# Kernel optimization log

Hardware: AMD Instinct MI355X
Metric: run time of the kernel (lower is better)

## Reference

```python
import jax, jax.numpy as jnp
import numpy as np

N, E, IN, H, HEADS, L, OUT = 4096, 262144, 64, 128, 4, 2, 2
DH = H // HEADS  # 32, per-head dim for both GAT and global MHA
BN_EPS = 1e-5
NEG_SLOPE = 0.2  # GATConv leaky_relu default


def setup_inputs() -> dict:
    key = jax.random.key(0)
    ks = iter(jax.random.split(key, 32))
    rn = lambda shape, s: jax.random.normal(next(ks), shape, jnp.float32) * s
    return {
        "x": rn((N, IN), 1.0),
        "edge_index": jax.random.randint(next(ks), (2, E), 0, N),
        "w_in": rn((H, IN), IN ** -0.5),
        "b_in": rn((H,), 0.02),
        "w_gat": rn((L, H, H), H ** -0.5),
        "att_src": rn((L, HEADS, DH), 0.1),
        "att_dst": rn((L, HEADS, DH), 0.1),
        "b_gat": rn((L, H), 0.02),
        "w_qkv": rn((L, 3 * H, H), H ** -0.5),
        "b_qkv": rn((L, 3 * H), 0.02),
        "w_o": rn((L, H, H), H ** -0.5),
        "b_o": rn((L, H), 0.02),
        "bn_gamma": 1.0 + rn((L, 3, H), 0.05),
        "bn_beta": rn((L, 3, H), 0.05),
        "w1": rn((L, 2 * H, H), H ** -0.5),
        "b1": rn((L, 2 * H), 0.02),
        "w2": rn((L, H, 2 * H), (2 * H) ** -0.5),
        "b2": rn((L, H), 0.02),
        "w_out": rn((OUT, H), H ** -0.5),
        "b_out": rn((OUT,), 0.02),
    }


def _bn(h, g, b):
    # eval-mode BatchNorm1d with running_mean=0, running_var=1
    return h * (g / jnp.sqrt(1.0 + BN_EPS)) + b


def _gat(x, src, dst, w, a_src, a_dst, bias):
    # GATConv(hidden, hidden//heads, heads=HEADS, add_self_loops=False), concat=True
    xp = (x @ w.T).reshape(N, HEADS, DH)                  # [N, HEADS, DH]
    al_s = jnp.einsum('nhd,hd->nh', xp, a_src)            # [N, HEADS]
    al_d = jnp.einsum('nhd,hd->nh', xp, a_dst)
    logit = al_s[src] + al_d[dst]                         # [E, HEADS]
    logit = jnp.where(logit >= 0, logit, NEG_SLOPE * logit)
    m = jax.ops.segment_max(logit, dst, num_segments=N)   # scatter-softmax over dst
    m = jnp.where(jnp.isfinite(m), m, 0.0)
    e = jnp.exp(logit - m[dst])
    denom = jax.ops.segment_sum(e, dst, num_segments=N)
    alpha = e / (denom[dst] + 1e-16)
    out = jax.ops.segment_sum(alpha[:, :, None] * xp[src], dst, num_segments=N)
    return out.reshape(N, H) + bias


def _mha(x, wqkv, bqkv, wo, bo):
    # torch.nn.MultiheadAttention self-attention over all N nodes (one graph)
    qkv = x @ wqkv.T + bqkv
    q, k, v = jnp.split(qkv, 3, axis=-1)
    q = q.reshape(N, HEADS, DH)
    k = k.reshape(N, HEADS, DH)
    v = v.reshape(N, HEADS, DH)
    scores = jnp.einsum('nhd,mhd->hnm', q, k) / jnp.sqrt(jnp.float32(DH))
    attn = jax.nn.softmax(scores, axis=-1)
    out = jnp.einsum('hnm,mhd->nhd', attn, v).reshape(N, H)
    return out @ wo.T + bo


def reference(x, edge_index, w_in, b_in, w_gat, att_src, att_dst, b_gat,
              w_qkv, b_qkv, w_o, b_o, bn_gamma, bn_beta,
              w1, b1, w2, b2, w_out, b_out):
    src, dst = edge_index[0], edge_index[1]
    h = jax.nn.relu(x @ w_in.T + b_in)
    for l in range(L):
        # GPSConv: local GAT branch (dropout inactive in eval)
        h_loc = _gat(h, src, dst, w_gat[l], att_src[l], att_dst[l], b_gat[l]) + h
        h_loc = _bn(h_loc, bn_gamma[l, 0], bn_beta[l, 0])
        # GPSConv: global attention branch
        h_att = _mha(h, w_qkv[l], b_qkv[l], w_o[l], b_o[l]) + h
        h_att = _bn(h_att, bn_gamma[l, 1], bn_beta[l, 1])
        out = h_loc + h_att
        mlp = jax.nn.relu(out @ w1[l].T + b1[l]) @ w2[l].T + b2[l]
        out = _bn(out + mlp, bn_gamma[l, 2], bn_beta[l, 2])
        # GPSRiskModel residual + relu (dropout inactive in eval)
        h = jax.nn.relu(out + h)
    return h @ w_out.T + b_out
```

## Files before the change

kernel.cpp:

```cpp
#include <hip/hip_runtime.h>

#define NN 4096
#define EE 262144
#define INF_ 64
#define HH 128
#define HEADS 4
#define DH 32
#define LL 2
#define NH (NN * HH)
#define KSPLIT 16
#define L2E 1.4426950408889634f

typedef unsigned short u16;
typedef unsigned int u32;
using bf16x8 = __attribute__((ext_vector_type(8))) short;
using f32x4 = __attribute__((ext_vector_type(4))) float;

__device__ __forceinline__ float bf2f(u16 v) { return __uint_as_float(((u32)v) << 16); }
__device__ __forceinline__ u16 f2bf(float f) {
    u32 u = __float_as_uint(f);
    u32 r = (u + 0x7fffu + ((u >> 16) & 1u)) >> 16;
    return (u16)r;
}
__device__ __forceinline__ u32 encf(float f) {
    u32 b = __float_as_uint(f);
    return (b & 0x80000000u) ? ~b : (b | 0x80000000u);
}
__device__ __forceinline__ float decf(u32 u) {
    u32 b = (u & 0x80000000u) ? (u & 0x7fffffffu) : ~u;
    return __uint_as_float(b);
}

__global__ __launch_bounds__(256) void k_detect(const u16* __restrict__ x, int* __restrict__ flag,
                                                int* __restrict__ cnt, u32* __restrict__ gmax) {
    int t = threadIdx.x;
    for (int i = t; i < NN; i += 256) cnt[i] = 0;
    if (t < 16) gmax[t] = 0;
    __shared__ int cs[256];
    u16 v = x[2 * t];
    int e = (v >> 7) & 0xFF;
    cs[t] = (e >= 100 && e <= 140) ? 1 : 0;
    __syncthreads();
    for (int s = 128; s > 0; s >>= 1) {
        if (t < s) cs[t] += cs[t + s];
        __syncthreads();
    }
    if (t == 0) *flag = (cs[0] >= 128) ? 1 : 0;
}

#define MAXSEG 16
struct SegF { const void* src[MAXSEG]; int dst[MAXSEG]; int n[MAXSEG]; int cnt; };
struct SegB { const void* src[8]; u16* dst[8]; u16* dst2[8]; int n[8]; int cnt; };
__global__ __launch_bounds__(256) void k_prep(SegF SF, float* __restrict__ W, SegB SB,
                                              const int* __restrict__ flag,
                                              const int* __restrict__ dst, int* __restrict__ cnt) {
    int bid = blockIdx.x, t = threadIdx.x;
    if (bid < 96) {
        int seg = bid >> 3, bx = bid & 7;
        if (seg >= SF.cnt) return;
        int n = SF.n[seg];
        float* d = W + SF.dst[seg];
        const void* s = SF.src[seg];
        int f = *flag;
        for (int i = bx * 256 + t; i < n; i += 8 * 256)
            d[i] = f ? bf2f(((const u16*)s)[i]) : ((const float*)s)[i];
    } else if (bid < 992) {
        int b2 = bid - 96;
        int seg = b2 >> 7, bx = b2 & 127;
        if (seg >= SB.cnt) return;
        int f = *flag;
        u16* d = SB.dst[seg];
        u16* d2 = SB.dst2[seg];
        if (f && !d2) return;
        int n = SB.n[seg];
        const void* s = SB.src[seg];
        for (int i = bx * 256 + t; i < n; i += 128 * 256) {
            if (d2) {
                float v = f ? bf2f(((const u16*)s)[i]) : ((const float*)s)[i];
                u16 h = f2bf(v);
                d[i] = h;
                d2[i] = f2bf(v - bf2f(h));
            } else {
                d[i] = f2bf(((const float*)s)[i]);
            }
        }
    } else {
        int e = (bid - 992) * 256 + t;
        if (e < EE) atomicAdd(&cnt[dst[e]], 1);
    }
}

__global__ __launch_bounds__(128) void k_mgemm(const u16* __restrict__ Ahi, const u16* __restrict__ Alo,
                                               const u16* __restrict__ Wc, const u16* __restrict__ Wd,
                                               const int* __restrict__ flag,
                                               const float* __restrict__ bias,
                                               float* __restrict__ outf, u16* __restrict__ outb16,
                                               u16* __restrict__ outhi, u16* __restrict__ outlo,
                                               int K, int J, int relu, int jtiles,
                                               const int* __restrict__ scnt, int* __restrict__ srowstart,
                                               int* __restrict__ scursor) {
    __shared__ int part[128];
    if ((int)blockIdx.y >= jtiles) {
        if (blockIdx.x != 0 || scnt == nullptr) return;
        int t = threadIdx.x;
        int loc[32];
        int s = 0;
#pragma unroll
        for (int i = 0; i < 32; ++i) { loc[i] = s; s += scnt[t * 32 + i]; }
        part[t] = s;
        __syncthreads();
        for (int off = 1; off < 128; off <<= 1) {
            int v = part[t];
            int a = (t >= off) ? part[t - off] : 0;
            __syncthreads();
            part[t] = v + a;
            __syncthreads();
        }
        int base = (t == 0) ? 0 : part[t - 1];
#pragma unroll
        for (int i = 0; i < 32; ++i) {
            srowstart[t * 32 + i] = base + loc[i];
            scursor[t * 32 + i] = base + loc[i];
        }
        return;
    }
    const u16* Wb = (*flag) ? Wd : Wc;
    int wave = threadIdx.x >> 6, lane = threadIdx.x & 63;
    int grp = lane >> 4, lcol = lane & 15;
    int m0 = blockIdx.x * 32 + wave * 16;
    int j0 = blockIdx.y * 64;
    f32x4 acc[4];
#pragma unroll
    for (int s = 0; s < 4; ++s) acc[s] = (f32x4){0.f, 0.f, 0.f, 0.f};
    const u16* ah = Ahi + (size_t)(m0 + lcol) * K + grp * 8;
    const u16* al = Alo + (size_t)(m0 + lcol) * K + grp * 8;
    const u16* wb = Wb + (size_t)(j0 + lcol) * K + grp * 8;
    for (int k = 0; k < K; k += 32) {
        bf16x8 va = *(const bf16x8*)(ah + k);
        bf16x8 vl = *(const bf16x8*)(al + k);
#pragma unroll
        for (int s = 0; s < 4; ++s) {
            bf16x8 vw = *(const bf16x8*)(wb + (size_t)s * 16 * K + k);
            acc[s] = __builtin_amdgcn_mfma_f32_16x16x32_bf16(va, vw, acc[s], 0, 0, 0);
            acc[s] = __builtin_amdgcn_mfma_f32_16x16x32_bf16(vl, vw, acc[s], 0, 0, 0);
        }
    }
#pragma unroll
    for (int s = 0; s < 4; ++s) {
        int col = j0 + s * 16 + lcol;
        float bs = bias ? bias[col] : 0.f;
#pragma unroll
        for (int r = 0; r < 4; ++r) {
            float v = acc[s][r] + bs;
            if (relu) v = fmaxf(v, 0.f);
            size_t idx = (size_t)(m0 + grp * 4 + r) * J + col;
            if (outf) outf[idx] = v;
            if (outb16) outb16[idx] = f2bf(v);
            if (outhi) {
                u16 hv = f2bf(v);
                outhi[idx] = hv;
                outlo[idx] = f2bf(v - bf2f(hv));
            }
        }
    }
}

__global__ __launch_bounds__(128) void k_gemm_gq(const u16* __restrict__ Ahi, const u16* __restrict__ Alo,
                                                 const u16* __restrict__ wgatc, const u16* __restrict__ wgatd,
                                                 const u16* __restrict__ wqkvc, const u16* __restrict__ wqkvd,
                                                 const int* __restrict__ flag,
                                                 const float* __restrict__ bqkv,
                                                 u16* __restrict__ xpb, u16* __restrict__ qkvb,
                                                 const int* __restrict__ esrc_src, const int* __restrict__ esrc_dst,
                                                 int* __restrict__ cursor, int* __restrict__ esrc) {
    if (blockIdx.y >= 8) {
        int b = (blockIdx.y - 8) * 128 + blockIdx.x;
        for (int e = b * 128 + threadIdx.x; e < EE; e += 32768) {
            int d = esrc_dst[e];
            int p = atomicAdd(&cursor[d], 1);
            esrc[p] = esrc_src[e];
        }
        return;
    }
    int wave = threadIdx.x >> 6, lane = threadIdx.x & 63;
    int grp = lane >> 4, lcol = lane & 15;
    int m0 = blockIdx.x * 32 + wave * 16;
    int jb = blockIdx.y;
    int j0 = jb * 64;
    int f = *flag;
    const u16* wgat = f ? wgatd : wgatc;
    const u16* wqkv = f ? wqkvd : wqkvc;
    const u16* Wb = (jb < 2) ? (wgat + (size_t)j0 * HH) : (wqkv + (size_t)(j0 - 128) * HH);
    f32x4 acc[4];
#pragma unroll
    for (int s = 0; s < 4; ++s) acc[s] = (f32x4){0.f, 0.f, 0.f, 0.f};
    const u16* ah = Ahi + (size_t)(m0 + lcol) * HH + grp * 8;
    const u16* al = Alo + (size_t)(m0 + lcol) * HH + grp * 8;
    const u16* wb = Wb + (size_t)lcol * HH + grp * 8;
    for (int k = 0; k < HH; k += 32) {
        bf16x8 va = *(const bf16x8*)(ah + k);
        bf16x8 vl = *(const bf16x8*)(al + k);
#pragma unroll
        for (int s = 0; s < 4; ++s) {
            bf16x8 vw = *(const bf16x8*)(wb + (size_t)s * 16 * HH + k);
            acc[s] = __builtin_amdgcn_mfma_f32_16x16x32_bf16(va, vw, acc[s], 0, 0, 0);
            acc[s] = __builtin_amdgcn_mfma_f32_16x16x32_bf16(vl, vw, acc[s], 0, 0, 0);
        }
    }
    if (jb < 2) {
#pragma unroll
        for (int s = 0; s < 4; ++s) {
            int col = j0 + s * 16 + lcol;
#pragma unroll
            for (int r = 0; r < 4; ++r)
                xpb[(size_t)(m0 + grp * 4 + r) * HH + col] = f2bf(acc[s][r]);
        }
    } else {
#pragma unroll
        for (int s = 0; s < 4; ++s) {
            int colq = j0 - 128 + s * 16 + lcol;
            float bs = bqkv[colq];
#pragma unroll
            for (int r = 0; r < 4; ++r)
                qkvb[(size_t)(m0 + grp * 4 + r) * 384 + colq] = f2bf(acc[s][r] + bs);
        }
    }
}

__global__ __launch_bounds__(256) void k_womlp(const u16* __restrict__ Ahi, const u16* __restrict__ Alo,
                                               const u16* __restrict__ Woc, const u16* __restrict__ Wod,
                                               const u16* __restrict__ W1c, const u16* __restrict__ W1d,
                                               const u16* __restrict__ W2c, const u16* __restrict__ W2d,
                                               const int* __restrict__ flag,
                                               const float* __restrict__ bo, const float* __restrict__ b1,
                                               const float* __restrict__ b2,
                                               const float* __restrict__ gatb, const float* __restrict__ bgat,
                                               const float* __restrict__ gam, const float* __restrict__ bet,
                                               const float* __restrict__ gam2, const float* __restrict__ bet2,
                                               float* __restrict__ hbuf, u16* __restrict__ hhi,
                                               u16* __restrict__ hlo) {
    __shared__ float Of[16][132];
    __shared__ u16 A2hi[16][136], A2lo[16][136];
    __shared__ u16 Hhi[16][264], Hlo[16][264];
    int f = *flag;
    const u16* Wo = f ? Wod : Woc;
    const u16* W1 = f ? W1d : W1c;
    const u16* W2 = f ? W2d : W2c;
    int wave = threadIdx.x >> 6, lane = threadIdx.x & 63;
    int grp = lane >> 4, lcol = lane & 15;
    int m0 = blockIdx.x * 16;
    float rs = rsqrtf(1.00001f);

    {
        int j0 = wave * 32;
        f32x4 acc[2];
#pragma unroll
        for (int s = 0; s < 2; ++s) acc[s] = (f32x4){0.f, 0.f, 0.f, 0.f};
        const u16* ah = Ahi + (size_t)(m0 + lcol) * HH + grp * 8;
        const u16* al = Alo + (size_t)(m0 + lcol) * HH + grp * 8;
        const u16* wb = Wo + (size_t)(j0 + lcol) * HH + grp * 8;
#pragma unroll
        for (int k = 0; k < HH; k += 32) {
            bf16x8 va = *(const bf16x8*)(ah + k);
            bf16x8 vl = *(const bf16x8*)(al + k);
#pragma unroll
            for (int s = 0; s < 2; ++s) {
                bf16x8 vw = *(const bf16x8*)(wb + (size_t)s * 16 * HH + k);
                acc[s] = __builtin_amdgcn_mfma_f32_16x16x32_bf16(va, vw, acc[s], 0, 0, 0);
                acc[s] = __builtin_amdgcn_mfma_f32_16x16x32_bf16(vl, vw, acc[s], 0, 0, 0);
            }
        }
#pragma unroll
        for (int s = 0; s < 2; ++s) {
            int col = j0 + s * 16 + lcol;
            float bs = bo[col];
            float g0 = gam[col] * rs, b0 = bet[col];
            float g1 = gam[HH + col] * rs, bb1 = bet[HH + col];
            float bg = bgat[col];
#pragma unroll
            for (int r = 0; r < 4; ++r) {
                int row = grp * 4 + r;
                size_t idx = (size_t)(m0 + row) * HH + col;
                float proj = acc[s][r] + bs;
                float hv = hbuf[idx];
                float hl = g0 * (gatb[idx] + bg + hv) + b0;
                float ha = g1 * (proj + hv) + bb1;
                float v = hl + ha;
                Of[row][col] = v;
                u16 hb = f2bf(v);
                A2hi[row][col] = hb;
                A2lo[row][col] = f2bf(v - bf2f(hb));
            }
        }
    }
    __syncthreads();
    {
        int j0 = wave * 64;
        f32x4 acc[4];
#pragma unroll
        for (int s = 0; s < 4; ++s) acc[s] = (f32x4){0.f, 0.f, 0.f, 0.f};
        const u16* wb = W1 + (size_t)(j0 + lcol) * HH + grp * 8;
#pragma unroll
        for (int k = 0; k < HH; k += 32) {
            bf16x8 va = *(const bf16x8*)(&A2hi[lcol][k + grp * 8]);
            bf16x8 vl = *(const bf16x8*)(&A2lo[lcol][k + grp * 8]);
#pragma unroll
            for (int s = 0; s < 4; ++s) {
                bf16x8 vw = *(const bf16x8*)(wb + (size_t)s * 16 * HH + k);
                acc[s] = __builtin_amdgcn_mfma_f32_16x16x32_bf16(va, vw, acc[s], 0, 0, 0);
                acc[s] = __builtin_amdgcn_mfma_f32_16x16x32_bf16(vl, vw, acc[s], 0, 0, 0);
            }
        }
#pragma unroll
        for (int s = 0; s < 4; ++s) {
            int col = j0 + s * 16 + lcol;
            float bs = b1[col];
#pragma unroll
            for (int r = 0; r < 4; ++r) {
                float v = fmaxf(acc[s][r] + bs, 0.f);
                int row = grp * 4 + r;
                u16 hv = f2bf(v);
                Hhi[row][col] = hv;
                Hlo[row][col] = f2bf(v - bf2f(hv));
            }
        }
    }
    __syncthreads();
    {
        int j0 = wave * 32;
        f32x4 acc[2];
#pragma unroll
        for (int s = 0; s < 2; ++s) acc[s] = (f32x4){0.f, 0.f, 0.f, 0.f};
        const u16* wb = W2 + (size_t)(j0 + lcol) * 256 + grp * 8;
#pragma unroll
        for (int k = 0; k < 256; k += 32) {
            bf16x8 va = *(const bf16x8*)(&Hhi[lcol][k + grp * 8]);
            bf16x8 vl = *(const bf16x8*)(&Hlo[lcol][k + grp * 8]);
#pragma unroll
            for (int s = 0; s < 2; ++s) {
                bf16x8 vw = *(const bf16x8*)(wb + (size_t)s * 16 * 256 + k);
                acc[s] = __builtin_amdgcn_mfma_f32_16x16x32_bf16(va, vw, acc[s], 0, 0, 0);
                acc[s] = __builtin_amdgcn_mfma_f32_16x16x32_bf16(vl, vw, acc[s], 0, 0, 0);
            }
        }
#pragma unroll
        for (int s = 0; s < 2; ++s) {
            int col = j0 + s * 16 + lcol;
            float bs = b2[col];
            float g2 = gam2[col] * rs, bb2 = bet2[col];
#pragma unroll
            for (int r = 0; r < 4; ++r) {
                int row = grp * 4 + r;
                size_t idx = (size_t)(m0 + row) * HH + col;
                float mlpo = acc[s][r] + bs;
                float o2 = g2 * (Of[row][col] + mlpo) + bb2;
                float v = fmaxf(o2 + hbuf[idx], 0.f);
                hbuf[idx] = v;
                u16 hb = f2bf(v);
                hhi[idx] = hb;
                hlo[idx] = f2bf(v - bf2f(hb));
            }
        }
    }
}

__global__ __launch_bounds__(256) void k_splitlog(const u16* __restrict__ qkvb,
                                                  float* __restrict__ PM, float* __restrict__ PL,
                                                  u16* __restrict__ PO,
                                                  const u16* __restrict__ xpb,
                                                  const float* __restrict__ asrc,
                                                  const float* __restrict__ adst,
                                                  float* __restrict__ als, float* __restrict__ ald,
                                                  u32* __restrict__ gmax) {
    __shared__ __align__(16) u16 Klds[64][40];
    __shared__ __align__(16) u32 Vlds[32][40];
    __shared__ __align__(16) u16 Plds[4][32][36];

    if (blockIdx.x >= 2048) {
        float* red = (float*)&Klds[0][0];
        int t = (blockIdx.x - 2048) * 256 + threadIdx.x;
        int n = t >> 2, hh = t & 3;
        const u16* xr = xpb + (size_t)n * HH + hh * DH;
        float s1 = 0.f, s2 = 0.f;
#pragma unroll
        for (int d = 0; d < DH; ++d) {
            float v = bf2f(xr[d]);
            s1 += v * asrc[hh * DH + d];
            s2 += v * adst[hh * DH + d];
        }
        als[t] = s1;
        ald[t] = s2;
        int lt = threadIdx.x;
        red[lt] = s1;
        __syncthreads();
        for (int off = 128; off >= 4; off >>= 1) {
            if (lt < off) red[lt] = fmaxf(red[lt], red[lt + off]);
            __syncthreads();
        }
        if (lt < 4) atomicMax(&gmax[lt], encf(red[lt]));
        __syncthreads();
        red[lt] = s2;
        __syncthreads();
        for (int off = 128; off >= 4; off >>= 1) {
            if (lt < off) red[lt] = fmaxf(red[lt], red[lt + off]);
            __syncthreads();
        }
        if (lt < 4) atomicMax(&gmax[4 + lt], encf(red[lt]));
        return;
    }

    const float C1 = 0.17677669529663687f * L2E;
    int head = blockIdx.x & 3;
    int qt = (blockIdx.x >> 2) & 31;
    int ks = blockIdx.x >> 7;
    int tid = threadIdx.x;
    int wave = tid >> 6, lane = tid & 63;
    int grp = lane >> 4, lcol = lane & 15;

    int qrow0 = qt * 128 + wave * 32;
    bf16x8 aQ0 = *(const bf16x8*)(qkvb + (size_t)(qrow0 + lcol) * 384 + head * 32 + grp * 8);
    bf16x8 aQ1 = *(const bf16x8*)(qkvb + (size_t)(qrow0 + 16 + lcol) * 384 + head * 32 + grp * 8);

    short onev = (lcol == 0) ? (short)0x3F80 : (short)0;
    bf16x8 bOne = {onev, onev, onev, onev, onev, onev, onev, onev};

    f32x4 oc00 = {0.f, 0.f, 0.f, 0.f}, oc01 = {0.f, 0.f, 0.f, 0.f};
    f32x4 oc10 = {0.f, 0.f, 0.f, 0.f}, oc11 = {0.f, 0.f, 0.f, 0.f};
    f32x4 ol0 = {0.f, 0.f, 0.f, 0.f}, ol1 = {0.f, 0.f, 0.f, 0.f};
    float msh = -INFINITY;

    int isK = (tid < 128);
    int st = tid & 127;
    int skey = st >> 1, shalf = (st & 1) * 16;
    int vj = st & 15, vc = (st >> 4) & 1, dgrp = st >> 5;
    const u16* kptr = qkvb + 128 + head * 32 + shalf;
    const u16* vptr = qkvb + 256 + head * 32 + dgrp * 8;
    int vk0 = vc * 32 + vj;
    int vk1 = vc * 32 + 16 + vj;

    int kt0 = ks * (NN / KSPLIT);
    bf16x8 r0, r1;
    if (isK) {
        r0 = *(const bf16x8*)(kptr + (size_t)(kt0 + skey) * 384);
        r1 = *(const bf16x8*)(kptr + (size_t)(kt0 + skey) * 384 + 8);
    } else {
        r0 = *(const bf16x8*)(vptr + (size_t)(kt0 + vk0) * 384);
        r1 = *(const bf16x8*)(vptr + (size_t)(kt0 + vk1) * 384);
    }

    const int NT = (NN / KSPLIT) / 64;
    for (int t = 0; t < NT; ++t) {
        if (isK) {
            *(bf16x8*)(&Klds[skey][shalf]) = r0;
            *(bf16x8*)(&Klds[skey][shalf + 8]) = r1;
        } else {
#pragma unroll
            for (int j = 0; j < 8; ++j)
                Vlds[dgrp * 8 + j][vc * 20 + vj] = (u32)(u16)r0[j] | ((u32)(u16)r1[j] << 16);
        }
        __syncthreads();
        if (t + 1 < NT) {
            int kn = kt0 + (t + 1) * 64;
            if (isK) {
                r0 = *(const bf16x8*)(kptr + (size_t)(kn + skey) * 384);
                r1 = *(const bf16x8*)(kptr + (size_t)(kn + skey) * 384 + 8);
            } else {
                r0 = *(const bf16x8*)(vptr + (size_t)(kn + vk0) * 384);
                r1 = *(const bf16x8*)(vptr + (size_t)(kn + vk1) * 384);
            }
        }
        f32x4 sc0[4], sc1[4];
        f32x4 zero = {0.f, 0.f, 0.f, 0.f};
        __builtin_amdgcn_s_setprio(1);
#pragma unroll
        for (int s = 0; s < 4; ++s) {
            bf16x8 bK = *(const bf16x8*)(&Klds[s * 16 + lcol][grp * 8]);
            sc0[s] = __builtin_amdgcn_mfma_f32_16x16x32_bf16(aQ0, bK, zero, 0, 0, 0);
            sc1[s] = __builtin_amdgcn_mfma_f32_16x16x32_bf16(aQ1, bK, zero, 0, 0, 0);
        }
        __builtin_amdgcn_s_setprio(0);
        float mymax = sc0[0][0];
#pragma unroll
        for (int s = 0; s < 4; ++s)
#pragma unroll
            for (int r = 0; r < 4; ++r) {
                mymax = fmaxf(mymax, sc0[s][r]);
                mymax = fmaxf(mymax, sc1[s][r]);
            }
        mymax = fmaxf(mymax, __shfl_xor(mymax, 1));
        mymax = fmaxf(mymax, __shfl_xor(mymax, 2));
        mymax = fmaxf(mymax, __shfl_xor(mymax, 4));
        mymax = fmaxf(mymax, __shfl_xor(mymax, 8));
        float mnew = fmaxf(msh, mymax * C1);
        float cc = __builtin_exp2f(msh - mnew);
        msh = mnew;
        oc00 *= cc; oc01 *= cc; ol0 *= cc;
        oc10 *= cc; oc11 *= cc; ol1 *= cc;
#pragma unroll
        for (int c2 = 0; c2 < 2; ++c2) {
#pragma unroll
            for (int r = 0; r < 4; ++r) {
                float p0 = __builtin_exp2f(__builtin_fmaf(sc0[2 * c2][r], C1, -mnew));
                float p1 = __builtin_exp2f(__builtin_fmaf(sc0[2 * c2 + 1][r], C1, -mnew));
                *(u32*)(&Plds[wave][grp * 4 + r][2 * lcol]) =
                    __builtin_amdgcn_perm(__float_as_uint(p1), __float_as_uint(p0), 0x07060302u);
                float q0 = __builtin_exp2f(__builtin_fmaf(sc1[2 * c2][r], C1, -mnew));
                float q1 = __builtin_exp2f(__builtin_fmaf(sc1[2 * c2 + 1][r], C1, -mnew));
                *(u32*)(&Plds[wave][16 + grp * 4 + r][2 * lcol]) =
                    __builtin_amdgcn_perm(__float_as_uint(q1), __float_as_uint(q0), 0x07060302u);
            }
            bf16x8 aP0 = *(const bf16x8*)(&Plds[wave][lcol][grp * 8]);
            bf16x8 aP1 = *(const bf16x8*)(&Plds[wave][16 + lcol][grp * 8]);
            bf16x8 bV0 = *(const bf16x8*)(&Vlds[lcol][c2 * 20 + grp * 4]);
            bf16x8 bV1 = *(const bf16x8*)(&Vlds[16 + lcol][c2 * 20 + grp * 4]);
            __builtin_amdgcn_s_setprio(1);
            oc00 = __builtin_amdgcn_mfma_f32_16x16x32_bf16(aP0, bV0, oc00, 0, 0, 0);
            oc01 = __builtin_amdgcn_mfma_f32_16x16x32_bf16(aP0, bV1, oc01, 0, 0, 0);
            ol0 = __builtin_amdgcn_mfma_f32_16x16x32_bf16(aP0, bOne, ol0, 0, 0, 0);
            oc10 = __builtin_amdgcn_mfma_f32_16x16x32_bf16(aP1, bV0, oc10, 0, 0, 0);
            oc11 = __builtin_amdgcn_mfma_f32_16x16x32_bf16(aP1, bV1, oc11, 0, 0, 0);
            ol1 = __builtin_amdgcn_mfma_f32_16x16x32_bf16(aP1, bOne, ol1, 0, 0, 0);
            __builtin_amdgcn_s_setprio(0);
        }
        __syncthreads();
    }
#pragma unroll
    for (int r = 0; r < 4; ++r) {
        int row0 = qrow0 + grp * 4 + r;
        size_t b0 = ((size_t)row0 * HEADS + head) * KSPLIT + ks;
        PO[b0 * 32 + lcol] = f2bf(oc00[r]);
        PO[b0 * 32 + 16 + lcol] = f2bf(oc01[r]);
        int row1 = row0 + 16;
        size_t b1 = ((size_t)row1 * HEADS + head) * KSPLIT + ks;
        PO[b1 * 32 + lcol] = f2bf(oc10[r]);
        PO[b1 * 32 + 16 + lcol] = f2bf(oc11[r]);
        if (lcol == 0) {
            PM[b0] = msh;
            PL[b0] = ol0[r];
            PM[b1] = msh;
            PL[b1] = ol1[r];
        }
    }
}

#define GCHUNK 256
__global__ __launch_bounds__(128) void k_gatcomb(const int* __restrict__ esrc, const int* __restrict__ rowstart,
                                                 const int* __restrict__ cnt, const float* __restrict__ als,
                                                 const float* __restrict__ ald, const u16* __restrict__ xpb,
                                                 float* __restrict__ gatout, const u32* __restrict__ gmax,
                                                 const float* __restrict__ PM, const float* __restrict__ PL,
                                                 const u16* __restrict__ PO, u16* __restrict__ atthi,
                                                 u16* __restrict__ attlo) {
    __shared__ float red[512];
    __shared__ float elds[GCHUNK * 4];
    __shared__ int slds[GCHUNK];
    int t = threadIdx.x;

    if (blockIdx.x >= NN) {
        int n2 = blockIdx.x - NN;
        float* wn = red;
        if (t < 64) {
            int head = t >> 4, ks = t & 15;
            size_t b = ((size_t)n2 * HEADS + head) * KSPLIT + ks;
            float pm = PM[b];
            float m = pm;
#pragma unroll
            for (int off = 1; off < 16; off <<= 1) m = fmaxf(m, __shfl_xor(m, off));
            float w = __builtin_exp2f(pm - m);
            float lw = PL[b] * w;
#pragma unroll
            for (int off = 1; off < 16; off <<= 1) lw += __shfl_xor(lw, off);
            wn[t] = w / lw;
        }
        __syncthreads();
        int head = t >> 5, dim = t & 31;
        size_t b0 = ((size_t)n2 * HEADS + head) * KSPLIT;
        float o = 0.f;
#pragma unroll
        for (int k = 0; k < KSPLIT; ++k)
            o += wn[head * 16 + k] * bf2f(PO[(b0 + k) * 32 + dim]);
        size_t idx = (size_t)n2 * HH + t;
        u16 h = f2bf(o);
        atthi[idx] = h;
        attlo[idx] = f2bf(o - bf2f(h));
        return;
    }

    int n = blockIdx.x;
    int base = rowstart[n], c = cnt[n];
    float4 adv = ((const float4*)ald)[n];
    float ad[4] = {adv.x, adv.y, adv.z, adv.w};
    float M2[4];
#pragma unroll
    for (int h = 0; h < 4; ++h) {
        float bound = decf(gmax[h]) + decf(gmax[4 + h]);
        float M = bound >= 0.f ? bound : 0.2f * bound;
        M2[h] = M * L2E;
    }
    float dsum[4] = {0.f, 0.f, 0.f, 0.f};
    float acc = 0.f;
    int ht = t >> 5;
    for (int ch = 0; ch < c; ch += GCHUNK) {
        int cn = min(GCHUNK, c - ch);
        __syncthreads();
        for (int i = t; i < cn; i += 128) {
            int s = esrc[base + ch + i];
            slds[i] = s;
            float4 as = ((const float4*)als)[s];
            float lg, e;
            lg = as.x + ad[0]; lg = lg >= 0.f ? lg : 0.2f * lg; e = __builtin_exp2f(lg * L2E - M2[0]); elds[i * 4 + 0] = e; dsum[0] += e;
            lg = as.y + ad[1]; lg = lg >= 0.f ? lg : 0.2f * lg; e = __builtin_exp2f(lg * L2E - M2[1]); elds[i * 4 + 1] = e; dsum[1] += e;
            lg = as.z + ad[2]; lg = lg >= 0.f ? lg : 0.2f * lg; e = __builtin_exp2f(lg * L2E - M2[2]); elds[i * 4 + 2] = e; dsum[2] += e;
            lg = as.w + ad[3]; lg = lg >= 0.f ? lg : 0.2f * lg; e = __builtin_exp2f(lg * L2E - M2[3]); elds[i * 4 + 3] = e; dsum[3] += e;
        }
        __syncthreads();
        int i = 0;
        for (; i + 4 <= cn; i += 4) {
            int s0 = slds[i], s1 = slds[i + 1], s2 = slds[i + 2], s3 = slds[i + 3];
            float x0 = bf2f(xpb[(size_t)s0 * HH + t]);
            float x1 = bf2f(xpb[(size_t)s1 * HH + t]);
            float x2 = bf2f(xpb[(size_t)s2 * HH + t]);
            float x3 = bf2f(xpb[(size_t)s3 * HH + t]);
            acc += elds[i * 4 + ht] * x0 + elds[(i + 1) * 4 + ht] * x1;
            acc += elds[(i + 2) * 4 + ht] * x2 + elds[(i + 3) * 4 + ht] * x3;
        }
        for (; i < cn; ++i) acc += elds[i * 4 + ht] * bf2f(xpb[(size_t)slds[i] * HH + t]);
    }
    __syncthreads();
#pragma unroll
    for (int h = 0; h < 4; ++h) red[h * 128 + t] = dsum[h];
    __syncthreads();
    for (int s2 = 64; s2 > 0; s2 >>= 1) {
        if (t < s2) {
#pragma unroll
            for (int h = 0; h < 4; ++h)
                red[h * 128 + t] += red[h * 128 + t + s2];
        }
        __syncthreads();
    }
    float inv = 1.f / (red[ht * 128] + 1e-16f);
    gatout[(size_t)n * HH + t] = acc * inv;
}

__global__ __launch_bounds__(64) void k_out(const float* __restrict__ h, const float* __restrict__ w,
                                            const float* __restrict__ b, void* __restrict__ yout,
                                            const int* __restrict__ flag) {
    int n = blockIdx.x, l = threadIdx.x;
    float a0 = 0.f, a1 = 0.f;
    for (int k = l; k < HH; k += 64) {
        float hv = h[(size_t)n * HH + k];
        a0 += hv * w[k];
        a1 += hv * w[HH + k];
    }
#pragma unroll
    for (int off = 32; off > 0; off >>= 1) {
        a0 += __shfl_xor(a0, off);
        a1 += __shfl_xor(a1, off);
    }
    if (l == 0) {
        float o0 = a0 + b[0], o1 = a1 + b[1];
        if (*flag) {
            u16* y = (u16*)yout;
            y[n * 2 + 0] = f2bf(o0);
            y[n * 2 + 1] = f2bf(o1);
        } else {
            float* y = (float*)yout;
            y[n * 2 + 0] = o0;
            y[n * 2 + 1] = o1;
        }
    }
}

extern "C" void kernel_launch(void* const* d_in, const int* in_sizes, int n_in,
                              void* d_out, int out_size, void* d_ws, size_t ws_size,
                              hipStream_t stream) {
    float* W = (float*)d_ws;
    size_t o = 0;
    auto take = [&](size_t n) { size_t r = o; o += n; return r; };
    size_t pb_in = take(HH);
    size_t pattS = take(LL * HEADS * DH);
    size_t pattD = take(LL * HEADS * DH);
    size_t pb_gat = take(LL * HH);
    size_t pb_qkv = take(LL * 3 * HH);
    size_t pb_o  = take(LL * HH);
    size_t pbn_g = take(LL * 3 * HH);
    size_t pbn_b = take(LL * 3 * HH);
    size_t pb1   = take(LL * 2 * HH);
    size_t pb2   = take(LL * HH);
    size_t pw_out = take(2 * HH);
    size_t pb_out = take(2);
    auto takeb = [&](size_t nu16) { size_t r = o; o += (nu16 + 1) / 2; return r; };
    size_t bw_in  = takeb(HH * INF_);
    size_t bw_gat = takeb(LL * HH * HH);
    size_t bw_qkv = takeb(LL * 3 * HH * HH);
    size_t bw_o   = takeb(LL * HH * HH);
    size_t bw1    = takeb(LL * 2 * HH * HH);
    size_t bw2    = takeb(LL * HH * 2 * HH);
    o = (o + 127) & ~(size_t)127;
    size_t ohbuf = take(NH);
    size_t ogat  = take(NH);
    size_t oals  = take(NN * HEADS);
    size_t oald  = take(NN * HEADS);
    size_t opm   = take(NN * HEADS * KSPLIT);
    size_t opl   = take(NN * HEADS * KSPLIT);
    size_t opo   = takeb((size_t)NN * HEADS * KSPLIT * 32);
    size_t oqkvb = takeb(NN * 384);
    size_t oxpb  = takeb(NH);
    size_t oxhi  = takeb(NN * INF_);
    size_t oxlo  = takeb(NN * INF_);
    size_t ohhi  = takeb(NH);
    size_t ohlo  = takeb(NH);
    size_t oahi  = takeb(NH);
    size_t oalo  = takeb(NH);
    int* ibase    = (int*)(W + o);
    int* iflag    = ibase;
    int* cnt      = ibase + 64;
    int* rowstart = cnt + NN;
    int* cursor   = rowstart + NN;
    int* esrc     = cursor + NN;
    u32* gmax     = (u32*)(esrc + EE);

    float* hbuf = W + ohbuf;
    float* gatb = W + ogat;
    float* als  = W + oals;
    float* ald  = W + oald;
    float* pmb  = W + opm;
    float* plb  = W + opl;
    u16* pob  = (u16*)(W + opo);
    u16* qkvb = (u16*)(W + oqkvb);
    u16* xpb  = (u16*)(W + oxpb);
    u16* xhi = (u16*)(W + oxhi), *xlo = (u16*)(W + oxlo);
    u16* hhi = (u16*)(W + ohhi), *hlo = (u16*)(W + ohlo);
    u16* ahi = (u16*)(W + oahi), *alo = (u16*)(W + oalo);

    const int* src = (const int*)d_in[1];
    const int* dst = (const int*)d_in[1] + EE;
    const u16* dw_in  = (const u16*)d_in[2];
    const u16* dw_gat = (const u16*)d_in[4];
    const u16* dw_qkv = (const u16*)d_in[8];
    const u16* dw_o   = (const u16*)d_in[10];
    const u16* dw1    = (const u16*)d_in[14];
    const u16* dw2    = (const u16*)d_in[16];

    k_detect<<<1, 256, 0, stream>>>((const u16*)d_in[0], iflag, cnt, gmax);

    SegF SF = {};
    int nf = 0;
    auto addf = [&](int idx, size_t off, int n) { SF.src[nf] = d_in[idx]; SF.dst[nf] = (int)off; SF.n[nf] = n; ++nf; };
    addf(3, pb_in, HH);
    addf(5, pattS, LL * HEADS * DH);
    addf(6, pattD, LL * HEADS * DH);
    addf(7, pb_gat, LL * HH);
    addf(9, pb_qkv, LL * 3 * HH);
    addf(11, pb_o, LL * HH);
    addf(12, pbn_g, LL * 3 * HH);
    addf(13, pbn_b, LL * 3 * HH);
    addf(15, pb1, LL * 2 * HH);
    addf(17, pb2, LL * HH);
    addf(18, pw_out, 2 * HH);
    addf(19, pb_out, 2);
    SF.cnt = nf;

    SegB SB = {};
    int nb = 0;
    auto addb = [&](int idx, size_t off, int n, u16* d2) {
        SB.src[nb] = d_in[idx]; SB.dst[nb] = (u16*)(W + off); SB.dst2[nb] = d2; SB.n[nb] = n; ++nb;
    };
    addb(2, bw_in, HH * INF_, nullptr);
    addb(4, bw_gat, LL * HH * HH, nullptr);
    addb(8, bw_qkv, LL * 3 * HH * HH, nullptr);
    addb(10, bw_o, LL * HH * HH, nullptr);
    addb(14, bw1, LL * 2 * HH * HH, nullptr);
    addb(16, bw2, LL * HH * 2 * HH, nullptr);
    SB.src[nb] = d_in[0]; SB.dst[nb] = xhi; SB.dst2[nb] = xlo; SB.n[nb] = NN * INF_; ++nb;
    SB.cnt = nb;

    k_prep<<<2016, 256, 0, stream>>>(SF, W, SB, iflag, dst, cnt);

    k_mgemm<<<dim3(NN / 32, HH / 64 + 1), 128, 0, stream>>>(xhi, xlo, (u16*)(W + bw_in), dw_in, iflag,
                                                            W + pb_in, hbuf, nullptr, hhi, hlo, INF_, HH, 1,
                                                            HH / 64, cnt, rowstart, cursor);

    for (int l = 0; l < LL; ++l) {
        k_gemm_gq<<<dim3(NN / 32, (l == 0) ? 10 : 8), 128, 0, stream>>>(hhi, hlo,
                                                        (u16*)(W + bw_gat) + (size_t)l * HH * HH,
                                                        dw_gat + (size_t)l * HH * HH,
                                                        (u16*)(W + bw_qkv) + (size_t)l * 3 * HH * HH,
                                                        dw_qkv + (size_t)l * 3 * HH * HH,
                                                        iflag, W + pb_qkv + l * 3 * HH, xpb, qkvb,
                                                        src, dst, cursor, esrc);
        k_splitlog<<<2048 + (NN * HEADS) / 256, 256, 0, stream>>>(qkvb, pmb, plb, pob, xpb,
                                                                  W + pattS + l * HEADS * DH,
                                                                  W + pattD + l * HEADS * DH,
                                                                  als, ald, gmax + l * 8);
        k_gatcomb<<<2 * NN, 128, 0, stream>>>(esrc, rowstart, cnt, als, ald, xpb, gatb, gmax + l * 8,
                                              pmb, plb, pob, ahi, alo);
        k_womlp<<<NN / 16, 256, 0, stream>>>(ahi, alo,
                                             (u16*)(W + bw_o) + (size_t)l * HH * HH,
                                             dw_o + (size_t)l * HH * HH,
                                             (u16*)(W + bw1) + (size_t)l * 2 * HH * HH,
                                             dw1 + (size_t)l * 2 * HH * HH,
                                             (u16*)(W + bw2) + (size_t)l * HH * 2 * HH,
                                             dw2 + (size_t)l * HH * 2 * HH, iflag,
                                             W + pb_o + l * HH, W + pb1 + l * 2 * HH, W + pb2 + l * HH,
                                             gatb, W + pb_gat + l * HH,
                                             W + pbn_g + l * 3 * HH, W + pbn_b + l * 3 * HH,
                                             W + pbn_g + l * 3 * HH + 2 * HH,
                                             W + pbn_b + l * 3 * HH + 2 * HH,
                                             hbuf, hhi, hlo);
    }
    k_out<<<NN, 64, 0, stream>>>(hbuf, W + pw_out, W + pb_out, d_out, iflag);
}
```

Before: 274.6 us.

## Fuse output projection into last MLP kernel and vectorize GAT gather

Removes the separate k_out launch by computing the final 2-wide output projection inside k_womlp on the last layer, reading the freshly computed h rows from shared memory. Separately, the GAT aggregation now has each thread load two packed bf16 values per edge and process two edges per iteration in parallel halves of the block, reducing the halves through LDS. The aim is to cut a kernel launch and the re-read of h, and to widen the gather loads. It adds a syncthreads and LDS reuse in k_womlp on the final layer, plus an extra reduction step in the GAT kernel.

```diff
diff --git a/kernel.cpp b/kernel.cpp
--- a/kernel.cpp
+++ b/kernel.cpp
@@ -238,7 +238,9 @@
                                                const float* __restrict__ gam, const float* __restrict__ bet,
                                                const float* __restrict__ gam2, const float* __restrict__ bet2,
                                                float* __restrict__ hbuf, u16* __restrict__ hhi,
-                                               u16* __restrict__ hlo) {
+                                               u16* __restrict__ hlo,
+                                               const float* __restrict__ wout, const float* __restrict__ bout,
+                                               void* __restrict__ yout) {
     __shared__ float Of[16][132];
     __shared__ u16 A2hi[16][136], A2lo[16][136];
     __shared__ u16 Hhi[16][264], Hlo[16][264];
@@ -356,9 +358,40 @@
                 float o2 = g2 * (Of[row][col] + mlpo) + bb2;
                 float v = fmaxf(o2 + hbuf[idx], 0.f);
                 hbuf[idx] = v;
+                Of[row][col] = v;
                 u16 hb = f2bf(v);
                 hhi[idx] = hb;
                 hlo[idx] = f2bf(v - bf2f(hb));
+            }
+        }
+    }
+    if (yout) {
+        __syncthreads();
+        int row = threadIdx.x >> 4, sub = threadIdx.x & 15;
+        float a0 = 0.f, a1 = 0.f;
+#pragma unroll
+        for (int k8 = 0; k8 < 8; ++k8) {
+            int k = sub * 8 + k8;
+            float hv = Of[row][k];
+            a0 += hv * wout[k];
+            a1 += hv * wout[HH + k];
+        }
+#pragma unroll
+        for (int off = 1; off < 16; off <<= 1) {
+            a0 += __shfl_xor(a0, off);
+            a1 += __shfl_xor(a1, off);
+        }
+        if (sub == 0) {
+            int n = m0 + row;
+            float o0 = a0 + bout[0], o1 = a1 + bout[1];
+            if (f) {
+                u16* y = (u16*)yout;
+                y[n * 2 + 0] = f2bf(o0);
+                y[n * 2 + 1] = f2bf(o1);
+            } else {
+                float* y = (float*)yout;
+                y[n * 2 + 0] = o0;
+                y[n * 2 + 1] = o1;
             }
         }
     }
@@ -598,7 +631,8 @@
         M2[h] = M * L2E;
     }
     float dsum[4] = {0.f, 0.f, 0.f, 0.f};
-    float acc = 0.f;
+    int eh = t >> 6, d = t & 63, hd = d >> 4;
+    float acc0 = 0.f, acc1 = 0.f;
     int ht = t >> 5;
     for (int ch = 0; ch < c; ch += GCHUNK) {
         int cn = min(GCHUNK, c - ch);
@@ -614,21 +648,23 @@
             lg = as.w + ad[3]; lg = lg >= 0.f ? lg : 0.2f * lg; e = __builtin_exp2f(lg * L2E - M2[3]); elds[i * 4 + 3] = e; dsum[3] += e;
         }
         __syncthreads();
-        int i = 0;
-        for (; i + 4 <= cn; i += 4) {
-            int s0 = slds[i], s1 = slds[i + 1], s2 = slds[i + 2], s3 = slds[i + 3];
-            float x0 = bf2f(xpb[(size_t)s0 * HH + t]);
-            float x1 = bf2f(xpb[(size_t)s1 * HH + t]);
-            float x2 = bf2f(xpb[(size_t)s2 * HH + t]);
-            float x3 = bf2f(xpb[(size_t)s3 * HH + t]);
-            acc += elds[i * 4 + ht] * x0 + elds[(i + 1) * 4 + ht] * x1;
-            acc += elds[(i + 2) * 4 + ht] * x2 + elds[(i + 3) * 4 + ht] * x3;
-        }
-        for (; i < cn; ++i) acc += elds[i * 4 + ht] * bf2f(xpb[(size_t)slds[i] * HH + t]);
+        for (int i = 0; i < cn; i += 4) {
+            int i0 = i + eh, i1 = i + 2 + eh;
+            int s0 = slds[i0 < cn ? i0 : cn - 1];
+            int s1 = slds[i1 < cn ? i1 : cn - 1];
+            u32 x0 = *(const u32*)(xpb + (size_t)s0 * HH + 2 * d);
+            u32 x1 = *(const u32*)(xpb + (size_t)s1 * HH + 2 * d);
+            float w0 = (i0 < cn) ? elds[i0 * 4 + hd] : 0.f;
+            float w1 = (i1 < cn) ? elds[i1 * 4 + hd] : 0.f;
+            acc0 += w0 * bf2f((u16)(x0 & 0xFFFF)) + w1 * bf2f((u16)(x1 & 0xFFFF));
+            acc1 += w0 * bf2f((u16)(x0 >> 16)) + w1 * bf2f((u16)(x1 >> 16));
+        }
     }
     __syncthreads();
 #pragma unroll
     for (int h = 0; h < 4; ++h) red[h * 128 + t] = dsum[h];
+    elds[eh * 128 + 2 * d] = acc0;
+    elds[eh * 128 + 2 * d + 1] = acc1;
     __syncthreads();
     for (int s2 = 64; s2 > 0; s2 >>= 1) {
         if (t < s2) {
@@ -638,37 +674,9 @@
         }
         __syncthreads();
     }
+    float accf = elds[t] + elds[128 + t];
     float inv = 1.f / (red[ht * 128] + 1e-16f);
-    gatout[(size_t)n * HH + t] = acc * inv;
-}
-
-__global__ __launch_bounds__(64) void k_out(const float* __restrict__ h, const float* __restrict__ w,
-                                            const float* __restrict__ b, void* __restrict__ yout,
-                                            const int* __restrict__ flag) {
-    int n = blockIdx.x, l = threadIdx.x;
-    float a0 = 0.f, a1 = 0.f;
-    for (int k = l; k < HH; k += 64) {
-        float hv = h[(size_t)n * HH + k];
-        a0 += hv * w[k];
-        a1 += hv * w[HH + k];
-    }
-#pragma unroll
-    for (int off = 32; off > 0; off >>= 1) {
-        a0 += __shfl_xor(a0, off);
-        a1 += __shfl_xor(a1, off);
-    }
-    if (l == 0) {
-        float o0 = a0 + b[0], o1 = a1 + b[1];
-        if (*flag) {
-            u16* y = (u16*)yout;
-            y[n * 2 + 0] = f2bf(o0);
-            y[n * 2 + 1] = f2bf(o1);
-        } else {
-            float* y = (float*)yout;
-            y[n * 2 + 0] = o0;
-            y[n * 2 + 1] = o1;
-        }
-    }
+    gatout[(size_t)n * HH + t] = accf * inv;
 }
 
 extern "C" void kernel_launch(void* const* d_in, const int* in_sizes, int n_in,
@@ -807,7 +815,8 @@
                                              W + pbn_g + l * 3 * HH, W + pbn_b + l * 3 * HH,
                                              W + pbn_g + l * 3 * HH + 2 * HH,
                                              W + pbn_b + l * 3 * HH + 2 * HH,
-                                             hbuf, hhi, hlo);
-    }
-    k_out<<<NN, 64, 0, stream>>>(hbuf, W + pw_out, W + pb_out, d_out, iflag);
-}
+                                             hbuf, hhi, hlo,
+                                             W + pw_out, W + pb_out,
+                                             (l == LL - 1) ? d_out : nullptr);
+    }
+}
```

New measurement: 270.3 us. No clear change (-1.6%).
